# Kernel tuning notes

Hardware: AMD Instinct MI355X
Metric: run time of the kernel (lower is better)

Reference implementation:

```python
import jax, jax.numpy as jnp
import numpy as np

NINP = 1024
NHID = 1024
BATCH = 16384


def setup_inputs() -> dict:
    key = jax.random.key(0)
    ks = jax.random.split(key, 12)
    std = 1.0 / np.sqrt(NHID)
    u = lambda k, shape: jax.random.uniform(k, shape, jnp.float32, -std, std)
    return {
        "x": jax.random.normal(ks[0], (BATCH, NINP), jnp.float32),
        "y": jax.random.normal(ks[1], (BATCH, NHID), jnp.float32),
        "z": jax.random.normal(ks[2], (BATCH, NHID), jnp.float32),
        "dt": jax.random.uniform(ks[3], (BATCH, 1), jnp.float32),
        "W_ih": u(ks[4], (4 * NHID, NINP)),
        "b_ih": u(ks[5], (4 * NHID,)),
        "W_hh": u(ks[6], (3 * NHID, NHID)),
        "b_hh": u(ks[7], (3 * NHID,)),
        "W_z": u(ks[8], (NHID, NHID)),
        "b_z": u(ks[9], (NHID,)),
        "W_dt": u(ks[10], (2, 1)),
        "b_dt": u(ks[11], (2,)),
    }


def reference(x, y, z, dt, W_ih, b_ih, W_hh, b_hh, W_z, b_z, W_dt, b_dt):
    # transformed_inp = inp2hid(x): [B, 4H]
    ti = x @ W_ih.T + b_ih
    # transformed_hid = hid2hid(y): [B, 3H]
    th = y @ W_hh.T + b_hh
    H = NHID
    i_dt1, i_dt2, i_z, i_y = ti[:, :H], ti[:, H:2*H], ti[:, 2*H:3*H], ti[:, 3*H:]
    h_dt1, h_dt2, h_y = th[:, :H], th[:, H:2*H], th[:, 2*H:]
    tdt = dt @ W_dt.T + b_dt  # [B, 2]
    t_dt1, t_dt2 = tdt[:, 0:1], tdt[:, 1:2]
    ms_dt_bar = jax.nn.sigmoid(t_dt1) * jax.nn.sigmoid(i_dt1 + h_dt1)
    ms_dt = jax.nn.sigmoid(t_dt2) * jax.nn.sigmoid(i_dt2 + h_dt2)
    z_new = (1.0 - ms_dt) * z + ms_dt * jnp.tanh(i_y + h_y)
    y_new = (1.0 - ms_dt_bar) * y + ms_dt_bar * jnp.tanh(z_new @ W_z.T + b_z + i_z)
    return (y_new, z_new)
```

## Files before the change

kernel.cpp:

```cpp
#include <hip/hip_runtime.h>
#include <hip/hip_bf16.h>

#define BATCH 16384
#define HDIM  1024
#define K1    2048

typedef __attribute__((ext_vector_type(4))) float f32x4;
typedef __attribute__((ext_vector_type(4))) int i32x4;

__device__ __forceinline__ unsigned short f2bf(float f) {
  union { float f; unsigned u; } v; v.f = f;
  unsigned r = v.u + 0x7FFFu + ((v.u >> 16) & 1u);
  return (unsigned short)(r >> 16);
}
__device__ __forceinline__ float bf2f(unsigned short h) {
  union { unsigned u; float f; } v; v.u = ((unsigned)h) << 16; return v.f;
}
__device__ __forceinline__ float sigmoidf_(float x) {
  return 1.0f / (1.0f + __builtin_amdgcn_exp2f(x * -1.4426950408889634f));
}
__device__ __forceinline__ float tanhf_(float x) {
  float xc = fminf(fmaxf(x, -8.0f), 8.0f);
  float e = __builtin_amdgcn_exp2f(xc * 2.8853900817779268f);
  return (e - 1.0f) / (e + 1.0f);
}
__device__ __forceinline__ void async16(const void* g, void* l) {
  __builtin_amdgcn_global_load_lds((const __attribute__((address_space(1))) void*)g,
                                   (__attribute__((address_space(3))) void*)l, 16, 0, 0);
}
__device__ __forceinline__ int q8p(float4 v, float s) {
  int a = __float2int_rn(fminf(fmaxf(v.x * s, -127.f), 127.f));
  int b = __float2int_rn(fminf(fmaxf(v.y * s, -127.f), 127.f));
  int c = __float2int_rn(fminf(fmaxf(v.z * s, -127.f), 127.f));
  int d = __float2int_rn(fminf(fmaxf(v.w * s, -127.f), 127.f));
  return (a & 255) | ((b & 255) << 8) | ((c & 255) << 16) | ((d & 255) << 24);
}

#define QXS (127.0f / 6.0f)
#define QWS (127.0f / 0.03125f)
#define SXW ((6.0f / 127.0f) * (0.03125f / 127.0f))

__global__ void k_conv(const float* __restrict__ x, const float* __restrict__ y,
                       const float* __restrict__ Wih, const float* __restrict__ Whh,
                       const float* __restrict__ Wz,
                       char* __restrict__ U8, char* __restrict__ W8,
                       char* __restrict__ Wz8) {
  const int stride = gridDim.x * blockDim.x;
  const int tid0 = blockIdx.x * blockDim.x + threadIdx.x;
  const int totalU = BATCH * (HDIM / 4);
  for (int q = tid0; q < totalU; q += stride) {
    int b = q >> 8;
    int c = (q & 255) << 2;
    float4 xv = *(const float4*)(x + (long)b * HDIM + c);
    float4 yv = *(const float4*)(y + (long)b * HDIM + c);
    *(int*)(U8 + (long)b * K1 + c) = q8p(xv, QXS);
    *(int*)(U8 + (long)b * K1 + HDIM + c) = q8p(yv, QXS);
  }
  const int totalW = 3072 * (K1 / 4);
  for (int q = tid0; q < totalW; q += stride) {
    int np = q >> 9;
    int kb = (q & 511) << 2;
    int bn = np / 192; int r = np - bn * 192;
    int w = r / 48; int r2 = r - w * 48;
    int c = r2 >> 4, i = r2 & 15;
    int h = bn * 64 + w * 16 + i;
    float4 v;
    if (kb < HDIM) {
      int row = (c == 0) ? h : (c == 1) ? (HDIM + h) : (3 * HDIM + h);
      v = *(const float4*)(Wih + (long)row * HDIM + kb);
    } else {
      int row = (c == 0) ? h : (c == 1) ? (HDIM + h) : (2 * HDIM + h);
      v = *(const float4*)(Whh + (long)row * HDIM + (kb - HDIM));
    }
    *(int*)(W8 + (long)np * K1 + kb) = q8p(v, QWS);
  }
  const int totalZ = HDIM * (K1 / 4);
  for (int q = tid0; q < totalZ; q += stride) {
    int n = q >> 9;
    int kb = (q & 511) << 2;
    float4 v = (kb < HDIM) ? *(const float4*)(Wz + (long)n * HDIM + kb)
                           : *(const float4*)(Wih + (long)(2 * HDIM + n) * HDIM + (kb - HDIM));
    *(int*)(Wz8 + (long)n * K1 + kb) = q8p(v, QWS);
  }
}

__global__ __launch_bounds__(512, 2) void k_gemm1(
    const char* __restrict__ U8, const char* __restrict__ W8,
    const float* __restrict__ z, const float* __restrict__ dtp,
    const float* __restrict__ bih, const float* __restrict__ bhh,
    const float* __restrict__ Wdt, const float* __restrict__ bdt,
    float* __restrict__ out, char* __restrict__ zn8,
    unsigned short* __restrict__ sbb) {
  __shared__ char lds[114688];
  char* ldsA = lds;
  char* ldsB = lds + 65536;
  const int bid = blockIdx.x;
  const int sid = (bid & 7) * 128 + (bid >> 3);
  const int bm = sid >> 4, bn = sid & 15;
  const long arow0 = (long)bm * 256, brow0 = (long)bn * 192;
  constexpr int NT = 32;

  const int t = threadIdx.x, lane = t & 63, wv = t >> 6;
  const int wm = wv >> 2, wn = wv & 3;
  const int rA = lane & 15;
  const int cphys = ((lane >> 4) << 4) ^ (((rA >> 1) & 3) << 4);
  const int t16 = t * 16;
  const bool blo = (t < 256);

  const int sA = t16 ^ (((t16 >> 7) & 3) << 4);
  const int rA0 = sA >> 6, cA0 = sA & 63;
  const char* pAa = U8 + (arow0 + rA0) * (long)K1 + cA0;
  const char* pAb = U8 + (arow0 + rA0 + 128) * (long)K1 + cA0;

  const int Lb0 = blo ? t16 : t16 + 4096;
  const int Lb1 = t16 + 4096;
  const int sB0 = Lb0 ^ (((Lb0 >> 7) & 3) << 4);
  const int sB1 = Lb1 ^ (((Lb1 >> 7) & 3) << 4);
  const char* pBg0 = W8 + (brow0 + (sB0 >> 6)) * (long)K1 + (sB0 & 63);
  const char* pBg1 = W8 + (brow0 + (sB1 >> 6)) * (long)K1 + (sB1 & 63);

  int offA[8], offB[3];
#pragma unroll
  for (int m = 0; m < 8; ++m)
    offA[m] = (wm * 128 + m * 16 + rA) * 64 + cphys;
#pragma unroll
  for (int n = 0; n < 3; ++n)
    offB[n] = (wn * 48 + n * 16 + rA) * 64 + cphys;

#define STAGE_(TT)                                                        \
  do {                                                                    \
    char* ab_ = ldsA + ((TT) & 3) * 16384;                                \
    char* bb_ = ldsB + ((TT) & 3) * 12288;                                \
    async16(pAa + (long)(TT) * 64, ab_ + t16);                            \
    async16(pAb + (long)(TT) * 64, ab_ + 8192 + t16);                     \
    async16(pBg0 + (long)(TT) * 64, bb_ + Lb0);                           \
    if (blo) async16(pBg1 + (long)(TT) * 64, bb_ + Lb1);                  \
  } while (0)
#define WSTEADY_                                                          \
  do {                                                                    \
    if (blo) asm volatile("s_waitcnt vmcnt(8) lgkmcnt(0)" ::: "memory");  \
    else     asm volatile("s_waitcnt vmcnt(6) lgkmcnt(0)" ::: "memory");  \
  } while (0)
#define WTAIL1_                                                           \
  do {                                                                    \
    if (blo) asm volatile("s_waitcnt vmcnt(4) lgkmcnt(0)" ::: "memory");  \
    else     asm volatile("s_waitcnt vmcnt(3) lgkmcnt(0)" ::: "memory");  \
  } while (0)
#define WTAIL0_ asm volatile("s_waitcnt vmcnt(0) lgkmcnt(0)" ::: "memory")
#define WLAST_  asm volatile("s_waitcnt lgkmcnt(0)" ::: "memory")

  i32x4 acc[8][3];
#pragma unroll
  for (int m = 0; m < 8; ++m)
#pragma unroll
    for (int n = 0; n < 3; ++n) acc[m][n] = (i32x4)(0);

  STAGE_(0);
  STAGE_(1);
  STAGE_(2);
  WSTEADY_;
  __builtin_amdgcn_s_barrier();

#pragma unroll 1
  for (int kt = 0; kt < NT; ++kt) {
    const char* Ab_ = ldsA + (kt & 3) * 16384;
    const char* Bb_ = ldsB + (kt & 3) * 12288;
    i32x4 af_[8], bf_[3];
#pragma unroll
    for (int m = 0; m < 8; ++m) af_[m] = *(const i32x4*)(Ab_ + offA[m]);
#pragma unroll
    for (int n = 0; n < 3; ++n) bf_[n] = *(const i32x4*)(Bb_ + offB[n]);
    if (kt < NT - 3) {
      STAGE_(kt + 3);
      WSTEADY_;
    } else if (kt == NT - 3) {
      WTAIL1_;
    } else if (kt == NT - 2) {
      WTAIL0_;
    } else {
      WLAST_;
    }
    __builtin_amdgcn_s_barrier();
    __builtin_amdgcn_sched_barrier(0);
    __builtin_amdgcn_s_setprio(1);
#pragma unroll
    for (int m = 0; m < 8; ++m)
#pragma unroll
      for (int n = 0; n < 3; ++n)
        acc[m][n] = __builtin_amdgcn_mfma_i32_16x16x64_i8(
            af_[m], bf_[n], acc[m][n], 0, 0, 0);
    __builtin_amdgcn_s_setprio(0);
  }
#undef STAGE_
#undef WSTEADY_
#undef WTAIL1_
#undef WTAIL0_
#undef WLAST_

  const int q4 = (lane >> 4) << 2;
  const int h = bn * 64 + wn * 16 + rA;
  const int rowbase = bm * 256 + wm * 128;
  const float bi0 = bih[h] + bhh[h];
  const float bi1 = bih[HDIM + h] + bhh[HDIM + h];
  const float bi2 = bih[3 * HDIM + h] + bhh[2 * HDIM + h];
  const float wdt0 = Wdt[0], wdt1 = Wdt[1], bdt0 = bdt[0], bdt1 = bdt[1];
#pragma unroll
  for (int m = 0; m < 8; ++m) {
#pragma unroll
    for (int j = 0; j < 4; ++j) {
      const int b = rowbase + m * 16 + q4 + j;
      const long idx = (long)b * HDIM + h;
      const float dv = dtp[b];
      const float s1 = sigmoidf_(dv * wdt0 + bdt0);
      const float s2 = sigmoidf_(dv * wdt1 + bdt1);
      const float g0 = (float)acc[m][0][j] * SXW + bi0;
      const float g1 = (float)acc[m][1][j] * SXW + bi1;
      const float g2 = (float)acc[m][2][j] * SXW + bi2;
      const float sbar = s1 * sigmoidf_(g0);
      const float s = s2 * sigmoidf_(g1);
      const float zt = tanhf_(g2);
      const float znew = (1.0f - s) * z[idx] + s * zt;
      out[(long)BATCH * HDIM + idx] = znew;
      int qz = __float2int_rn(fminf(fmaxf(znew * QXS, -127.f), 127.f));
      zn8[idx] = (char)qz;
      sbb[idx] = f2bf(sbar);
    }
  }
}

__global__ __launch_bounds__(512, 2) void k_gemm2(
    const char* __restrict__ Zn8, const char* __restrict__ U8,
    const char* __restrict__ Wz8, const unsigned short* __restrict__ sbb,
    const float* __restrict__ yin, const float* __restrict__ bz,
    float* __restrict__ out) {
  __shared__ char lds[98304];
  char* ldsA = lds;
  char* ldsB = lds + 65536;
  const int bid = blockIdx.x;
  const int sid = (bid & 7) * 64 + (bid >> 3);
  const int bm = sid >> 3, bn = sid & 7;
  const long arow0 = (long)bm * 256, brow0 = (long)bn * 128;
  constexpr int NT = 32, KSPLIT = 16;

  const int t = threadIdx.x, lane = t & 63, wv = t >> 6;
  const int wm = wv >> 2, wn = wv & 3;
  const int rA = lane & 15;
  const int cphys = ((lane >> 4) << 4) ^ (((rA >> 1) & 3) << 4);
  const int t16 = t * 16;

  const int sA = t16 ^ (((t16 >> 7) & 3) << 4);
  const int rA0 = sA >> 6, cA0 = sA & 63;
  const char* pZa = Zn8 + (arow0 + rA0) * (long)HDIM + cA0;
  const char* pZb = Zn8 + (arow0 + rA0 + 128) * (long)HDIM + cA0;
  const char* pXa = U8 + (arow0 + rA0) * (long)K1 + cA0;
  const char* pXb = U8 + (arow0 + rA0 + 128) * (long)K1 + cA0;

  const int sB0 = t16 ^ (((t16 >> 7) & 3) << 4);
  const char* pBg0 = Wz8 + (brow0 + (sB0 >> 6)) * (long)K1 + (sB0 & 63);

  int offA[8], offB[2];
#pragma unroll
  for (int m = 0; m < 8; ++m)
    offA[m] = (wm * 128 + m * 16 + rA) * 64 + cphys;
#pragma unroll
  for (int n = 0; n < 2; ++n)
    offB[n] = (wn * 32 + n * 16 + rA) * 64 + cphys;

#define STAGE2_(TT)                                                       \
  do {                                                                    \
    char* ab_ = ldsA + ((TT) & 3) * 16384;                                \
    char* bb_ = ldsB + ((TT) & 3) * 8192;                                 \
    if ((TT) < KSPLIT) {                                                  \
      async16(pZa + (long)(TT) * 64, ab_ + t16);                          \
      async16(pZb + (long)(TT) * 64, ab_ + 8192 + t16);                   \
    } else {                                                              \
      async16(pXa + (long)((TT) - KSPLIT) * 64, ab_ + t16);               \
      async16(pXb + (long)((TT) - KSPLIT) * 64, ab_ + 8192 + t16);        \
    }                                                                     \
    async16(pBg0 + (long)(TT) * 64, bb_ + t16);                           \
  } while (0)
#define W2S_ asm volatile("s_waitcnt vmcnt(6) lgkmcnt(0)" ::: "memory")
#define W2A_ asm volatile("s_waitcnt vmcnt(3) lgkmcnt(0)" ::: "memory")
#define W2B_ asm volatile("s_waitcnt vmcnt(0) lgkmcnt(0)" ::: "memory")
#define W2C_ asm volatile("s_waitcnt lgkmcnt(0)" ::: "memory")

  i32x4 acc[8][2];
#pragma unroll
  for (int m = 0; m < 8; ++m)
#pragma unroll
    for (int n = 0; n < 2; ++n) acc[m][n] = (i32x4)(0);

  STAGE2_(0);
  STAGE2_(1);
  STAGE2_(2);
  W2S_;
  __builtin_amdgcn_s_barrier();

#pragma unroll 1
  for (int kt = 0; kt < NT; ++kt) {
    const char* Ab_ = ldsA + (kt & 3) * 16384;
    const char* Bb_ = ldsB + (kt & 3) * 8192;
    i32x4 af_[8], bf_[2];
#pragma unroll
    for (int m = 0; m < 8; ++m) af_[m] = *(const i32x4*)(Ab_ + offA[m]);
#pragma unroll
    for (int n = 0; n < 2; ++n) bf_[n] = *(const i32x4*)(Bb_ + offB[n]);
    if (kt < NT - 3) {
      STAGE2_(kt + 3);
      W2S_;
    } else if (kt == NT - 3) {
      W2A_;
    } else if (kt == NT - 2) {
      W2B_;
    } else {
      W2C_;
    }
    __builtin_amdgcn_s_barrier();
    __builtin_amdgcn_sched_barrier(0);
    __builtin_amdgcn_s_setprio(1);
#pragma unroll
    for (int m = 0; m < 8; ++m)
#pragma unroll
      for (int n = 0; n < 2; ++n)
        acc[m][n] = __builtin_amdgcn_mfma_i32_16x16x64_i8(
            af_[m], bf_[n], acc[m][n], 0, 0, 0);
    __builtin_amdgcn_s_setprio(0);
  }
#undef STAGE2_
#undef W2S_
#undef W2A_
#undef W2B_
#undef W2C_

  const int q4 = (lane >> 4) << 2;
  const int rowbase = bm * 256 + wm * 128;
#pragma unroll
  for (int n = 0; n < 2; ++n) {
    const int hc = bn * 128 + wn * 32 + n * 16 + rA;
    const float bzv = bz[hc];
#pragma unroll
    for (int m = 0; m < 8; ++m) {
#pragma unroll
      for (int j = 0; j < 4; ++j) {
        const int b = rowbase + m * 16 + q4 + j;
        const long idx = (long)b * HDIM + hc;
        const float tv = tanhf_((float)acc[m][n][j] * SXW + bzv);
        const float sb = bf2f(sbb[idx]);
        out[idx] = (1.0f - sb) * yin[idx] + sb * tv;
      }
    }
  }
}

extern "C" void kernel_launch(void* const* d_in, const int* in_sizes, int n_in,
                              void* d_out, int out_size, void* d_ws, size_t ws_size,
                              hipStream_t stream) {
  const float* x   = (const float*)d_in[0];
  const float* y   = (const float*)d_in[1];
  const float* z   = (const float*)d_in[2];
  const float* dtp = (const float*)d_in[3];
  const float* Wih = (const float*)d_in[4];
  const float* bih = (const float*)d_in[5];
  const float* Whh = (const float*)d_in[6];
  const float* bhh = (const float*)d_in[7];
  const float* Wz  = (const float*)d_in[8];
  const float* bz  = (const float*)d_in[9];
  const float* Wdt = (const float*)d_in[10];
  const float* bdt = (const float*)d_in[11];

  char* ws = (char*)d_ws;
  char*           U8  = ws;
  char*           W8  = ws + 33554432;
  char*           Wz8 = ws + 39845888;
  char*           Zn8 = ws + 41943040;
  unsigned short* Sbb = (unsigned short*)(ws + 58720256);
  float* out = (float*)d_out;

  k_conv<<<2048, 256, 0, stream>>>(x, y, Wih, Whh, Wz, U8, W8, Wz8);
  k_gemm1<<<1024, 512, 0, stream>>>(U8, W8, z, dtp, bih, bhh, Wdt, bdt, out, Zn8, Sbb);
  k_gemm2<<<512, 512, 0, stream>>>(Zn8, U8, Wz8, Sbb, y, bz, out);
}
```

Baseline: 262.0 us.

## Shrink GEMM tiles and use three-stage LDS ring for higher occupancy

Both GEMM kernels switch from a four-stage LDS pipeline to a three-stage ring buffer with rotating read and stage pointers. The first GEMM's M tile is halved to 128 rows and its grid doubled, and the second GEMM's tile is reshaped from 256x128 to 128x256. Each block now needs less shared memory and fewer accumulators, and launch bounds request 4 blocks per CU, so more waves can hide memory latency. The cost is less data reuse per tile, a shallower prefetch pipeline, and a tighter per-thread register budget that may force spills.

```diff
diff --git a/kernel.cpp b/kernel.cpp
--- a/kernel.cpp
+++ b/kernel.cpp
@@ -84,20 +84,19 @@
   }
 }
 
-__global__ __launch_bounds__(512, 2) void k_gemm1(
+__global__ __launch_bounds__(512, 4) void k_gemm1(
     const char* __restrict__ U8, const char* __restrict__ W8,
     const float* __restrict__ z, const float* __restrict__ dtp,
     const float* __restrict__ bih, const float* __restrict__ bhh,
     const float* __restrict__ Wdt, const float* __restrict__ bdt,
     float* __restrict__ out, char* __restrict__ zn8,
     unsigned short* __restrict__ sbb) {
-  __shared__ char lds[114688];
-  char* ldsA = lds;
-  char* ldsB = lds + 65536;
+  __shared__ char lds[61440];
+  constexpr int TSZ = 20480;
   const int bid = blockIdx.x;
-  const int sid = (bid & 7) * 128 + (bid >> 3);
+  const int sid = (bid & 7) * 256 + (bid >> 3);
   const int bm = sid >> 4, bn = sid & 15;
-  const long arow0 = (long)bm * 256, brow0 = (long)bn * 192;
+  const long arow0 = (long)bm * 128, brow0 = (long)bn * 192;
   constexpr int NT = 32;
 
   const int t = threadIdx.x, lane = t & 63, wv = t >> 6;
@@ -108,9 +107,7 @@
   const bool blo = (t < 256);
 
   const int sA = t16 ^ (((t16 >> 7) & 3) << 4);
-  const int rA0 = sA >> 6, cA0 = sA & 63;
-  const char* pAa = U8 + (arow0 + rA0) * (long)K1 + cA0;
-  const char* pAb = U8 + (arow0 + rA0 + 128) * (long)K1 + cA0;
+  const char* pAa = U8 + (arow0 + (sA >> 6)) * (long)K1 + (sA & 63);
 
   const int Lb0 = blo ? t16 : t16 + 4096;
   const int Lb1 = t16 + 4096;
@@ -119,62 +116,53 @@
   const char* pBg0 = W8 + (brow0 + (sB0 >> 6)) * (long)K1 + (sB0 & 63);
   const char* pBg1 = W8 + (brow0 + (sB1 >> 6)) * (long)K1 + (sB1 & 63);
 
-  int offA[8], offB[3];
-#pragma unroll
-  for (int m = 0; m < 8; ++m)
-    offA[m] = (wm * 128 + m * 16 + rA) * 64 + cphys;
+  int offA[4], offB[3];
+#pragma unroll
+  for (int m = 0; m < 4; ++m)
+    offA[m] = (wm * 64 + m * 16 + rA) * 64 + cphys;
 #pragma unroll
   for (int n = 0; n < 3; ++n)
-    offB[n] = (wn * 48 + n * 16 + rA) * 64 + cphys;
-
-#define STAGE_(TT)                                                        \
+    offB[n] = 8192 + (wn * 48 + n * 16 + rA) * 64 + cphys;
+
+#define STAGE_(DST, TT)                                                   \
   do {                                                                    \
-    char* ab_ = ldsA + ((TT) & 3) * 16384;                                \
-    char* bb_ = ldsB + ((TT) & 3) * 12288;                                \
-    async16(pAa + (long)(TT) * 64, ab_ + t16);                            \
-    async16(pAb + (long)(TT) * 64, ab_ + 8192 + t16);                     \
-    async16(pBg0 + (long)(TT) * 64, bb_ + Lb0);                           \
-    if (blo) async16(pBg1 + (long)(TT) * 64, bb_ + Lb1);                  \
+    async16(pAa + (long)(TT) * 64, (DST) + t16);                          \
+    async16(pBg0 + (long)(TT) * 64, (DST) + 8192 + Lb0);                  \
+    if (blo) async16(pBg1 + (long)(TT) * 64, (DST) + 8192 + Lb1);         \
   } while (0)
 #define WSTEADY_                                                          \
   do {                                                                    \
-    if (blo) asm volatile("s_waitcnt vmcnt(8) lgkmcnt(0)" ::: "memory");  \
-    else     asm volatile("s_waitcnt vmcnt(6) lgkmcnt(0)" ::: "memory");  \
-  } while (0)
-#define WTAIL1_                                                           \
-  do {                                                                    \
-    if (blo) asm volatile("s_waitcnt vmcnt(4) lgkmcnt(0)" ::: "memory");  \
-    else     asm volatile("s_waitcnt vmcnt(3) lgkmcnt(0)" ::: "memory");  \
+    if (blo) asm volatile("s_waitcnt vmcnt(3) lgkmcnt(0)" ::: "memory");  \
+    else     asm volatile("s_waitcnt vmcnt(2) lgkmcnt(0)" ::: "memory");  \
   } while (0)
 #define WTAIL0_ asm volatile("s_waitcnt vmcnt(0) lgkmcnt(0)" ::: "memory")
 #define WLAST_  asm volatile("s_waitcnt lgkmcnt(0)" ::: "memory")
 
-  i32x4 acc[8][3];
-#pragma unroll
-  for (int m = 0; m < 8; ++m)
+  i32x4 acc[4][3];
+#pragma unroll
+  for (int m = 0; m < 4; ++m)
 #pragma unroll
     for (int n = 0; n < 3; ++n) acc[m][n] = (i32x4)(0);
 
-  STAGE_(0);
-  STAGE_(1);
-  STAGE_(2);
+  STAGE_(lds, 0);
+  STAGE_(lds + TSZ, 1);
   WSTEADY_;
   __builtin_amdgcn_s_barrier();
 
+  const char* rd = lds;
+  char* st = lds + 2 * TSZ;
+  const char* ldsend = lds + 3 * TSZ;
+
 #pragma unroll 1
   for (int kt = 0; kt < NT; ++kt) {
-    const char* Ab_ = ldsA + (kt & 3) * 16384;
-    const char* Bb_ = ldsB + (kt & 3) * 12288;
-    i32x4 af_[8], bf_[3];
-#pragma unroll
-    for (int m = 0; m < 8; ++m) af_[m] = *(const i32x4*)(Ab_ + offA[m]);
-#pragma unroll
-    for (int n = 0; n < 3; ++n) bf_[n] = *(const i32x4*)(Bb_ + offB[n]);
-    if (kt < NT - 3) {
-      STAGE_(kt + 3);
+    i32x4 af_[4], bf_[3];
+#pragma unroll
+    for (int m = 0; m < 4; ++m) af_[m] = *(const i32x4*)(rd + offA[m]);
+#pragma unroll
+    for (int n = 0; n < 3; ++n) bf_[n] = *(const i32x4*)(rd + offB[n]);
+    if (kt < NT - 2) {
+      STAGE_(st, kt + 2);
       WSTEADY_;
-    } else if (kt == NT - 3) {
-      WTAIL1_;
     } else if (kt == NT - 2) {
       WTAIL0_;
     } else {
@@ -184,28 +172,29 @@
     __builtin_amdgcn_sched_barrier(0);
     __builtin_amdgcn_s_setprio(1);
 #pragma unroll
-    for (int m = 0; m < 8; ++m)
+    for (int m = 0; m < 4; ++m)
 #pragma unroll
       for (int n = 0; n < 3; ++n)
         acc[m][n] = __builtin_amdgcn_mfma_i32_16x16x64_i8(
             af_[m], bf_[n], acc[m][n], 0, 0, 0);
     __builtin_amdgcn_s_setprio(0);
+    rd += TSZ; rd = (rd == ldsend) ? lds : rd;
+    st += TSZ; st = (st == ldsend) ? (char*)lds : st;
   }
 #undef STAGE_
 #undef WSTEADY_
-#undef WTAIL1_
 #undef WTAIL0_
 #undef WLAST_
 
   const int q4 = (lane >> 4) << 2;
   const int h = bn * 64 + wn * 16 + rA;
-  const int rowbase = bm * 256 + wm * 128;
+  const int rowbase = bm * 128 + wm * 64;
   const float bi0 = bih[h] + bhh[h];
   const float bi1 = bih[HDIM + h] + bhh[HDIM + h];
   const float bi2 = bih[3 * HDIM + h] + bhh[2 * HDIM + h];
   const float wdt0 = Wdt[0], wdt1 = Wdt[1], bdt0 = bdt[0], bdt1 = bdt[1];
 #pragma unroll
-  for (int m = 0; m < 8; ++m) {
+  for (int m = 0; m < 4; ++m) {
 #pragma unroll
     for (int j = 0; j < 4; ++j) {
       const int b = rowbase + m * 16 + q4 + j;
@@ -228,18 +217,17 @@
   }
 }
 
-__global__ __launch_bounds__(512, 2) void k_gemm2(
+__global__ __launch_bounds__(512, 4) void k_gemm2(
     const char* __restrict__ Zn8, const char* __restrict__ U8,
     const char* __restrict__ Wz8, const unsigned short* __restrict__ sbb,
     const float* __restrict__ yin, const float* __restrict__ bz,
     float* __restrict__ out) {
-  __shared__ char lds[98304];
-  char* ldsA = lds;
-  char* ldsB = lds + 65536;
+  __shared__ char lds[73728];
+  constexpr int TSZ = 24576;
   const int bid = blockIdx.x;
   const int sid = (bid & 7) * 64 + (bid >> 3);
-  const int bm = sid >> 3, bn = sid & 7;
-  const long arow0 = (long)bm * 256, brow0 = (long)bn * 128;
+  const int bm = sid >> 2, bn = sid & 3;
+  const long arow0 = (long)bm * 128, brow0 = (long)bn * 256;
   constexpr int NT = 32, KSPLIT = 16;
 
   const int t = threadIdx.x, lane = t & 63, wv = t >> 6;
@@ -249,67 +237,59 @@
   const int t16 = t * 16;
 
   const int sA = t16 ^ (((t16 >> 7) & 3) << 4);
-  const int rA0 = sA >> 6, cA0 = sA & 63;
-  const char* pZa = Zn8 + (arow0 + rA0) * (long)HDIM + cA0;
-  const char* pZb = Zn8 + (arow0 + rA0 + 128) * (long)HDIM + cA0;
-  const char* pXa = U8 + (arow0 + rA0) * (long)K1 + cA0;
-  const char* pXb = U8 + (arow0 + rA0 + 128) * (long)K1 + cA0;
-
-  const int sB0 = t16 ^ (((t16 >> 7) & 3) << 4);
+  const char* pZa = Zn8 + (arow0 + (sA >> 6)) * (long)HDIM + (sA & 63);
+  const char* pXa = U8 + (arow0 + (sA >> 6)) * (long)K1 + (sA & 63);
+
+  const int Lb0 = t16, Lb1 = t16 + 8192;
+  const int sB0 = Lb0 ^ (((Lb0 >> 7) & 3) << 4);
+  const int sB1 = Lb1 ^ (((Lb1 >> 7) & 3) << 4);
   const char* pBg0 = Wz8 + (brow0 + (sB0 >> 6)) * (long)K1 + (sB0 & 63);
-
-  int offA[8], offB[2];
-#pragma unroll
-  for (int m = 0; m < 8; ++m)
-    offA[m] = (wm * 128 + m * 16 + rA) * 64 + cphys;
-#pragma unroll
-  for (int n = 0; n < 2; ++n)
-    offB[n] = (wn * 32 + n * 16 + rA) * 64 + cphys;
-
-#define STAGE2_(TT)                                                       \
+  const char* pBg1 = Wz8 + (brow0 + (sB1 >> 6)) * (long)K1 + (sB1 & 63);
+
+  int offA[4], offB[4];
+#pragma unroll
+  for (int m = 0; m < 4; ++m)
+    offA[m] = (wm * 64 + m * 16 + rA) * 64 + cphys;
+#pragma unroll
+  for (int n = 0; n < 4; ++n)
+    offB[n] = 8192 + (wn * 64 + n * 16 + rA) * 64 + cphys;
+
+#define STAGE2_(DST, TT)                                                  \
   do {                                                                    \
-    char* ab_ = ldsA + ((TT) & 3) * 16384;                                \
-    char* bb_ = ldsB + ((TT) & 3) * 8192;                                 \
-    if ((TT) < KSPLIT) {                                                  \
-      async16(pZa + (long)(TT) * 64, ab_ + t16);                          \
-      async16(pZb + (long)(TT) * 64, ab_ + 8192 + t16);                   \
-    } else {                                                              \
-      async16(pXa + (long)((TT) - KSPLIT) * 64, ab_ + t16);               \
-      async16(pXb + (long)((TT) - KSPLIT) * 64, ab_ + 8192 + t16);        \
-    }                                                                     \
-    async16(pBg0 + (long)(TT) * 64, bb_ + t16);                           \
+    if ((TT) < KSPLIT) async16(pZa + (long)(TT) * 64, (DST) + t16);       \
+    else async16(pXa + (long)((TT) - KSPLIT) * 64, (DST) + t16);          \
+    async16(pBg0 + (long)(TT) * 64, (DST) + 8192 + Lb0);                  \
+    async16(pBg1 + (long)(TT) * 64, (DST) + 8192 + Lb1);                  \
   } while (0)
-#define W2S_ asm volatile("s_waitcnt vmcnt(6) lgkmcnt(0)" ::: "memory")
-#define W2A_ asm volatile("s_waitcnt vmcnt(3) lgkmcnt(0)" ::: "memory")
+#define W2S_ asm volatile("s_waitcnt vmcnt(3) lgkmcnt(0)" ::: "memory")
 #define W2B_ asm volatile("s_waitcnt vmcnt(0) lgkmcnt(0)" ::: "memory")
 #define W2C_ asm volatile("s_waitcnt lgkmcnt(0)" ::: "memory")
 
-  i32x4 acc[8][2];
-#pragma unroll
-  for (int m = 0; m < 8; ++m)
-#pragma unroll
-    for (int n = 0; n < 2; ++n) acc[m][n] = (i32x4)(0);
-
-  STAGE2_(0);
-  STAGE2_(1);
-  STAGE2_(2);
+  i32x4 acc[4][4];
+#pragma unroll
+  for (int m = 0; m < 4; ++m)
+#pragma unroll
+    for (int n = 0; n < 4; ++n) acc[m][n] = (i32x4)(0);
+
+  STAGE2_(lds, 0);
+  STAGE2_(lds + TSZ, 1);
   W2S_;
   __builtin_amdgcn_s_barrier();
 
+  const char* rd = lds;
+  char* st = lds + 2 * TSZ;
+  const char* ldsend = lds + 3 * TSZ;
+
 #pragma unroll 1
   for (int kt = 0; kt < NT; ++kt) {
-    const char* Ab_ = ldsA + (kt & 3) * 16384;
-    const char* Bb_ = ldsB + (kt & 3) * 8192;
-    i32x4 af_[8], bf_[2];
-#pragma unroll
-    for (int m = 0; m < 8; ++m) af_[m] = *(const i32x4*)(Ab_ + offA[m]);
-#pragma unroll
-    for (int n = 0; n < 2; ++n) bf_[n] = *(const i32x4*)(Bb_ + offB[n]);
-    if (kt < NT - 3) {
-      STAGE2_(kt + 3);
+    i32x4 af_[4], bf_[4];
+#pragma unroll
+    for (int m = 0; m < 4; ++m) af_[m] = *(const i32x4*)(rd + offA[m]);
+#pragma unroll
+    for (int n = 0; n < 4; ++n) bf_[n] = *(const i32x4*)(rd + offB[n]);
+    if (kt < NT - 2) {
+      STAGE2_(st, kt + 2);
       W2S_;
-    } else if (kt == NT - 3) {
-      W2A_;
     } else if (kt == NT - 2) {
       W2B_;
     } else {
@@ -319,27 +299,28 @@
     __builtin_amdgcn_sched_barrier(0);
     __builtin_amdgcn_s_setprio(1);
 #pragma unroll
-    for (int m = 0; m < 8; ++m)
-#pragma unroll
-      for (int n = 0; n < 2; ++n)
+    for (int m = 0; m < 4; ++m)
+#pragma unroll
+      for (int n = 0; n < 4; ++n)
         acc[m][n] = __builtin_amdgcn_mfma_i32_16x16x64_i8(
             af_[m], bf_[n], acc[m][n], 0, 0, 0);
     __builtin_amdgcn_s_setprio(0);
+    rd += TSZ; rd = (rd == ldsend) ? lds : rd;
+    st += TSZ; st = (st == ldsend) ? (char*)lds : st;
   }
 #undef STAGE2_
 #undef W2S_
-#undef W2A_
 #undef W2B_
 #undef W2C_
 
   const int q4 = (lane >> 4) << 2;
-  const int rowbase = bm * 256 + wm * 128;
-#pragma unroll
-  for (int n = 0; n < 2; ++n) {
-    const int hc = bn * 128 + wn * 32 + n * 16 + rA;
+  const int rowbase = bm * 128 + wm * 64;
+#pragma unroll
+  for (int n = 0; n < 4; ++n) {
+    const int hc = bn * 256 + wn * 64 + n * 16 + rA;
     const float bzv = bz[hc];
 #pragma unroll
-    for (int m = 0; m < 8; ++m) {
+    for (int m = 0; m < 4; ++m) {
 #pragma unroll
       for (int j = 0; j < 4; ++j) {
         const int b = rowbase + m * 16 + q4 + j;
@@ -377,6 +358,6 @@
   float* out = (float*)d_out;
 
   k_conv<<<2048, 256, 0, stream>>>(x, y, Wih, Whh, Wz, U8, W8, Wz8);
-  k_gemm1<<<1024, 512, 0, stream>>>(U8, W8, z, dtp, bih, bhh, Wdt, bdt, out, Zn8, Sbb);
+  k_gemm1<<<2048, 512, 0, stream>>>(U8, W8, z, dtp, bih, bhh, Wdt, bdt, out, Zn8, Sbb);
   k_gemm2<<<512, 512, 0, stream>>>(Zn8, U8, Wz8, Sbb, y, bz, out);
 }
```

New measurement: 296.8 us. 13.3% more time.

## Halve gemm1 M-tile and use triple-buffered LDS ring for higher occupancy

Applied to the files above, without the earlier changes.

Shrinks the first int8 GEMM's block tile from 256 to 128 rows, doubling the grid, and cuts the LDS pipeline from four stages to a three-slot ring of combined A/B tiles. Shared memory per block drops from about 112KB to 60KB and the accumulator count halves, so launch bounds ask for four blocks per CU instead of two. The goal is more resident waves to hide memory latency. In exchange the per-block arithmetic intensity is lower, the same W8 tiles are re-read by twice as many blocks, and the prefetch distance shrinks by one stage.

```diff
diff --git a/kernel.cpp b/kernel.cpp
--- a/kernel.cpp
+++ b/kernel.cpp
@@ -84,20 +84,19 @@
   }
 }
 
-__global__ __launch_bounds__(512, 2) void k_gemm1(
+__global__ __launch_bounds__(512, 4) void k_gemm1(
     const char* __restrict__ U8, const char* __restrict__ W8,
     const float* __restrict__ z, const float* __restrict__ dtp,
     const float* __restrict__ bih, const float* __restrict__ bhh,
     const float* __restrict__ Wdt, const float* __restrict__ bdt,
     float* __restrict__ out, char* __restrict__ zn8,
     unsigned short* __restrict__ sbb) {
-  __shared__ char lds[114688];
-  char* ldsA = lds;
-  char* ldsB = lds + 65536;
+  __shared__ char lds[61440];
+  constexpr int TSZ = 20480;
   const int bid = blockIdx.x;
-  const int sid = (bid & 7) * 128 + (bid >> 3);
+  const int sid = (bid & 7) * 256 + (bid >> 3);
   const int bm = sid >> 4, bn = sid & 15;
-  const long arow0 = (long)bm * 256, brow0 = (long)bn * 192;
+  const long arow0 = (long)bm * 128, brow0 = (long)bn * 192;
   constexpr int NT = 32;
 
   const int t = threadIdx.x, lane = t & 63, wv = t >> 6;
@@ -108,9 +107,7 @@
   const bool blo = (t < 256);
 
   const int sA = t16 ^ (((t16 >> 7) & 3) << 4);
-  const int rA0 = sA >> 6, cA0 = sA & 63;
-  const char* pAa = U8 + (arow0 + rA0) * (long)K1 + cA0;
-  const char* pAb = U8 + (arow0 + rA0 + 128) * (long)K1 + cA0;
+  const char* pAa = U8 + (arow0 + (sA >> 6)) * (long)K1 + (sA & 63);
 
   const int Lb0 = blo ? t16 : t16 + 4096;
   const int Lb1 = t16 + 4096;
@@ -119,62 +116,53 @@
   const char* pBg0 = W8 + (brow0 + (sB0 >> 6)) * (long)K1 + (sB0 & 63);
   const char* pBg1 = W8 + (brow0 + (sB1 >> 6)) * (long)K1 + (sB1 & 63);
 
-  int offA[8], offB[3];
-#pragma unroll
-  for (int m = 0; m < 8; ++m)
-    offA[m] = (wm * 128 + m * 16 + rA) * 64 + cphys;
+  int offA[4], offB[3];
+#pragma unroll
+  for (int m = 0; m < 4; ++m)
+    offA[m] = (wm * 64 + m * 16 + rA) * 64 + cphys;
 #pragma unroll
   for (int n = 0; n < 3; ++n)
-    offB[n] = (wn * 48 + n * 16 + rA) * 64 + cphys;
-
-#define STAGE_(TT)                                                        \
+    offB[n] = 8192 + (wn * 48 + n * 16 + rA) * 64 + cphys;
+
+#define STAGE_(DST, TT)                                                   \
   do {                                                                    \
-    char* ab_ = ldsA + ((TT) & 3) * 16384;                                \
-    char* bb_ = ldsB + ((TT) & 3) * 12288;                                \
-    async16(pAa + (long)(TT) * 64, ab_ + t16);                            \
-    async16(pAb + (long)(TT) * 64, ab_ + 8192 + t16);                     \
-    async16(pBg0 + (long)(TT) * 64, bb_ + Lb0);                           \
-    if (blo) async16(pBg1 + (long)(TT) * 64, bb_ + Lb1);                  \
+    async16(pAa + (long)(TT) * 64, (DST) + t16);                          \
+    async16(pBg0 + (long)(TT) * 64, (DST) + 8192 + Lb0);                  \
+    if (blo) async16(pBg1 + (long)(TT) * 64, (DST) + 8192 + Lb1);         \
   } while (0)
 #define WSTEADY_                                                          \
   do {                                                                    \
-    if (blo) asm volatile("s_waitcnt vmcnt(8) lgkmcnt(0)" ::: "memory");  \
-    else     asm volatile("s_waitcnt vmcnt(6) lgkmcnt(0)" ::: "memory");  \
-  } while (0)
-#define WTAIL1_                                                           \
-  do {                                                                    \
-    if (blo) asm volatile("s_waitcnt vmcnt(4) lgkmcnt(0)" ::: "memory");  \
-    else     asm volatile("s_waitcnt vmcnt(3) lgkmcnt(0)" ::: "memory");  \
+    if (blo) asm volatile("s_waitcnt vmcnt(3) lgkmcnt(0)" ::: "memory");  \
+    else     asm volatile("s_waitcnt vmcnt(2) lgkmcnt(0)" ::: "memory");  \
   } while (0)
 #define WTAIL0_ asm volatile("s_waitcnt vmcnt(0) lgkmcnt(0)" ::: "memory")
 #define WLAST_  asm volatile("s_waitcnt lgkmcnt(0)" ::: "memory")
 
-  i32x4 acc[8][3];
-#pragma unroll
-  for (int m = 0; m < 8; ++m)
+  i32x4 acc[4][3];
+#pragma unroll
+  for (int m = 0; m < 4; ++m)
 #pragma unroll
     for (int n = 0; n < 3; ++n) acc[m][n] = (i32x4)(0);
 
-  STAGE_(0);
-  STAGE_(1);
-  STAGE_(2);
+  STAGE_(lds, 0);
+  STAGE_(lds + TSZ, 1);
   WSTEADY_;
   __builtin_amdgcn_s_barrier();
 
+  const char* rd = lds;
+  char* st = lds + 2 * TSZ;
+  const char* ldsend = lds + 3 * TSZ;
+
 #pragma unroll 1
   for (int kt = 0; kt < NT; ++kt) {
-    const char* Ab_ = ldsA + (kt & 3) * 16384;
-    const char* Bb_ = ldsB + (kt & 3) * 12288;
-    i32x4 af_[8], bf_[3];
-#pragma unroll
-    for (int m = 0; m < 8; ++m) af_[m] = *(const i32x4*)(Ab_ + offA[m]);
-#pragma unroll
-    for (int n = 0; n < 3; ++n) bf_[n] = *(const i32x4*)(Bb_ + offB[n]);
-    if (kt < NT - 3) {
-      STAGE_(kt + 3);
+    i32x4 af_[4], bf_[3];
+#pragma unroll
+    for (int m = 0; m < 4; ++m) af_[m] = *(const i32x4*)(rd + offA[m]);
+#pragma unroll
+    for (int n = 0; n < 3; ++n) bf_[n] = *(const i32x4*)(rd + offB[n]);
+    if (kt < NT - 2) {
+      STAGE_(st, kt + 2);
       WSTEADY_;
-    } else if (kt == NT - 3) {
-      WTAIL1_;
     } else if (kt == NT - 2) {
       WTAIL0_;
     } else {
@@ -184,28 +172,29 @@
     __builtin_amdgcn_sched_barrier(0);
     __builtin_amdgcn_s_setprio(1);
 #pragma unroll
-    for (int m = 0; m < 8; ++m)
+    for (int m = 0; m < 4; ++m)
 #pragma unroll
       for (int n = 0; n < 3; ++n)
         acc[m][n] = __builtin_amdgcn_mfma_i32_16x16x64_i8(
             af_[m], bf_[n], acc[m][n], 0, 0, 0);
     __builtin_amdgcn_s_setprio(0);
+    rd += TSZ; rd = (rd == ldsend) ? lds : rd;
+    st += TSZ; st = (st == ldsend) ? (char*)lds : st;
   }
 #undef STAGE_
 #undef WSTEADY_
-#undef WTAIL1_
 #undef WTAIL0_
 #undef WLAST_
 
   const int q4 = (lane >> 4) << 2;
   const int h = bn * 64 + wn * 16 + rA;
-  const int rowbase = bm * 256 + wm * 128;
+  const int rowbase = bm * 128 + wm * 64;
   const float bi0 = bih[h] + bhh[h];
   const float bi1 = bih[HDIM + h] + bhh[HDIM + h];
   const float bi2 = bih[3 * HDIM + h] + bhh[2 * HDIM + h];
   const float wdt0 = Wdt[0], wdt1 = Wdt[1], bdt0 = bdt[0], bdt1 = bdt[1];
 #pragma unroll
-  for (int m = 0; m < 8; ++m) {
+  for (int m = 0; m < 4; ++m) {
 #pragma unroll
     for (int j = 0; j < 4; ++j) {
       const int b = rowbase + m * 16 + q4 + j;
@@ -377,6 +366,6 @@
   float* out = (float*)d_out;
 
   k_conv<<<2048, 256, 0, stream>>>(x, y, Wih, Whh, Wz, U8, W8, Wz8);
-  k_gemm1<<<1024, 512, 0, stream>>>(U8, W8, z, dtp, bih, bhh, Wdt, bdt, out, Zn8, Sbb);
+  k_gemm1<<<2048, 512, 0, stream>>>(U8, W8, z, dtp, bih, bhh, Wdt, bdt, out, Zn8, Sbb);
   k_gemm2<<<512, 512, 0, stream>>>(Zn8, U8, Wz8, Sbb, y, bz, out);
 }
```

Result: slower. 267.6 us (+2.2%).
